# Optimization experiments

Measured on AMD Instinct MI355X. Metric: run time of the kernel, lower is better.

The kernel has to match this reference:

```python
import jax, jax.numpy as jnp
import numpy as np

B, S, D, H, DH = 2, 2048, 1024, 16, 64
LN_EPS = 1e-5

def _layernorm(x, g, b):
    mu = jnp.mean(x, axis=-1, keepdims=True)
    var = jnp.mean(jnp.square(x - mu), axis=-1, keepdims=True)
    return (x - mu) * jax.lax.rsqrt(var + LN_EPS) * g + b

def setup_inputs() -> dict:
    key = jax.random.key(0)
    ks = jax.random.split(key, 12)
    s = 0.02
    return {
        'x': jax.random.normal(ks[0], (B, S, D), jnp.float32),
        'attention_mask': jnp.zeros((B, S), jnp.bool_),
        'Wq': jax.random.normal(ks[1], (H, D, DH), jnp.float32) * s,
        'bq': jnp.zeros((H, DH), jnp.float32),
        'Wk': jax.random.normal(ks[2], (H, D, DH), jnp.float32) * s,
        'bk': jnp.zeros((H, DH), jnp.float32),
        'Wv': jax.random.normal(ks[3], (H, D, DH), jnp.float32) * s,
        'bv': jnp.zeros((H, DH), jnp.float32),
        'ln_g': jnp.ones((D,), jnp.float32),
        'ln_b': jnp.zeros((D,), jnp.float32),
        'W1': jax.random.normal(ks[4], (D, 4 * D), jnp.float32) * s,
        'b1': jnp.zeros((4 * D,), jnp.float32),
        'W2': jax.random.normal(ks[5], (4 * D, D), jnp.float32) * s,
        'b2': jnp.zeros((D,), jnp.float32),
    }

def reference(x, attention_mask, Wq, bq, Wk, bk, Wv, bv, ln_g, ln_b, W1, b1, W2, b2):
    # NOTE: source has a typo bug ('attentoin_score'), so the attention_mask is
    # computed-then-discarded; softmax is applied to the UNMASKED scaled scores.
    dh = Wq.shape[-1]
    q = jnp.einsum('bsd,hde->bhse', x, Wq) + bq[:, None, :]  # [B,H,S,dh]
    k = jnp.einsum('bsd,hde->bhse', x, Wk) + bk[:, None, :]
    v = jnp.einsum('bsd,hde->bhse', x, Wv) + bv[:, None, :]
    scores = jnp.einsum('bhse,bhte->bhst', q, k) / jnp.sqrt(jnp.float32(dh))
    attn = jax.nn.softmax(scores, axis=-1)
    o = jnp.einsum('bhst,bhte->bhse', attn, v)  # [B,H,S,dh]
    b_, h_, s_, e_ = o.shape
    # concat heads along last dim == transpose then reshape
    mha = jnp.transpose(o, (0, 2, 1, 3)).reshape(b_, s_, h_ * e_)
    h1 = _layernorm(x + mha, ln_g, ln_b)
    ffn = jax.nn.relu(h1 @ W1 + b1) @ W2 + b2
    return _layernorm(h1 + ffn, ln_g, ln_b)
```

## Files before the change

### kernel.cpp

```cpp
#include <hip/hip_runtime.h>

#define DEVI __device__ __forceinline__

typedef __attribute__((ext_vector_type(8))) __bf16 bf16x8;
typedef __attribute__((ext_vector_type(4))) float f32x4;
typedef __attribute__((ext_vector_type(4))) unsigned short u16x4;
typedef __attribute__((ext_vector_type(8))) unsigned short u16x8;

static DEVI unsigned short f2bf(float f) {
  unsigned int i = __float_as_uint(f);
  i += 0x7fffu + ((i >> 16) & 1u);
  return (unsigned short)(i >> 16);
}

static DEVI unsigned short f2bfh(float f) {
  union { __bf16 h; unsigned short u; } c;
  c.h = (__bf16)f;
  return c.u;
}

static DEVI f32x4 mfma16x16x32(bf16x8 a, bf16x8 b, f32x4 c) {
  return __builtin_amdgcn_mfma_f32_16x16x32_bf16(a, b, c, 0, 0, 0);
}

static DEVI void async_ld16(const void* g, void* lds) {
  __builtin_amdgcn_global_load_lds(
      (const __attribute__((address_space(1))) void*)g,
      (__attribute__((address_space(3))) void*)lds, 16, 0, 0);
}

template <int BN, int OUT_MODE, bool RELU>
static DEVI void gemm_bt_core(const unsigned short* __restrict__ A, int lda,
                              const unsigned short* __restrict__ Bt, int ldb,
                              int K, int m0, int n0,
                              const float* __restrict__ bias,
                              void* __restrict__ Cp, int ldc,
                              const float* __restrict__ bq,
                              const float* __restrict__ bk,
                              const float* __restrict__ bv,
                              unsigned short* __restrict__ qo,
                              unsigned short* __restrict__ ko,
                              unsigned short* __restrict__ vo) {
  constexpr int MT = (BN == 128) ? 4 : 2;
  constexpr int NT = 4;
  __shared__ __align__(16) unsigned short As[128 * 32];
  __shared__ __align__(16) unsigned short Bs[BN * 32];

  const int tid = threadIdx.x;
  const int w = tid >> 6, l = tid & 63;
  const int lr = l & 15, lq = l >> 4;
  const int wm0 = (BN == 128) ? ((w >> 1) * 64) : (w * 32);
  const int wn0 = (BN == 128) ? ((w & 1) * 64) : 0;
  const int lrow = l >> 2;
  const int lcol = (l & 3) * 8;

  f32x4 acc[MT][NT];
#pragma unroll
  for (int i = 0; i < MT; ++i)
#pragma unroll
    for (int j = 0; j < NT; ++j) acc[i][j] = (f32x4){0.f, 0.f, 0.f, 0.f};

  for (int kb = 0; kb < K; kb += 32) {
#pragma unroll
    for (int p = 0; p < 2; ++p) {
      const int r0 = p * 64 + w * 16;
      async_ld16(A + (size_t)(m0 + r0 + lrow) * lda + kb + lcol, As + r0 * 32);
    }
#pragma unroll
    for (int p = 0; p < BN / 64; ++p) {
      const int r0 = p * 64 + w * 16;
      async_ld16(Bt + (size_t)(n0 + r0 + lrow) * ldb + kb + lcol, Bs + r0 * 32);
    }
    __syncthreads();

    bf16x8 af[MT], bfr[NT];
#pragma unroll
    for (int mt = 0; mt < MT; ++mt)
      af[mt] = *(const bf16x8*)(As + (wm0 + mt * 16 + lr) * 32 + lq * 8);
#pragma unroll
    for (int nt = 0; nt < NT; ++nt)
      bfr[nt] = *(const bf16x8*)(Bs + (wn0 + nt * 16 + lr) * 32 + lq * 8);
#pragma unroll
    for (int mt = 0; mt < MT; ++mt)
#pragma unroll
      for (int nt = 0; nt < NT; ++nt)
        acc[mt][nt] = mfma16x16x32(af[mt], bfr[nt], acc[mt][nt]);
    __syncthreads();
  }

#pragma unroll
  for (int mt = 0; mt < MT; ++mt) {
    const int grow = m0 + wm0 + mt * 16 + lq * 4;
#pragma unroll
    for (int nt = 0; nt < NT; ++nt) {
      const int gcol = n0 + wn0 + nt * 16 + lr;
      if (OUT_MODE == 2) {
        const int which = gcol >> 10;
        const int h = (gcol >> 6) & 15;
        const int e = gcol & 63;
        const float* bp = (which == 0) ? bq : (which == 1) ? bk : bv;
        const float bvv = bp[gcol & 1023];
        unsigned short* op = (which == 0) ? qo : (which == 1) ? ko : vo;
#pragma unroll
        for (int r = 0; r < 4; ++r) {
          const int row = grow + r;
          const int b_ = row >> 11, s_ = row & 2047;
          const size_t base = (size_t)((b_ << 4) + h) * 131072 + (size_t)s_ * 64;
          if (which == 1) {
            const int o = e >> 3;
            const int pos = (((o ^ (s_ & 7)) << 3) | (e & 7));
            op[base + pos] = f2bf((acc[mt][nt][r] + bvv) * 0.18033688011112f);
          } else {
            op[base + e] = f2bf(acc[mt][nt][r] + bvv);
          }
        }
      } else if (OUT_MODE == 3) {
#pragma unroll
        for (int r = 0; r < 4; ++r)
          ((unsigned short*)Cp)[(size_t)(grow + r) * ldc + gcol] =
              f2bf(acc[mt][nt][r]);
      } else {
        const float bvv = bias[gcol];
#pragma unroll
        for (int r = 0; r < 4; ++r) {
          float val = acc[mt][nt][r] + bvv;
          if (RELU) val = fmaxf(val, 0.f);
          if (OUT_MODE == 1)
            ((unsigned short*)Cp)[(size_t)(grow + r) * ldc + gcol] = f2bf(val);
          else
            ((float*)Cp)[(size_t)(grow + r) * ldc + gcol] = val;
        }
      }
    }
  }
}

__global__ __launch_bounds__(256) void k_gemm_qkv(
    const unsigned short* __restrict__ xb, const unsigned short* __restrict__ Wt,
    const float* __restrict__ bq, const float* __restrict__ bk,
    const float* __restrict__ bv, unsigned short* __restrict__ qo,
    unsigned short* __restrict__ ko, unsigned short* __restrict__ vo) {
  gemm_bt_core<128, 2, false>(xb, 1024, Wt, 1024, 1024, blockIdx.x * 128,
                              blockIdx.y * 128, nullptr, nullptr, 0, bq, bk, bv,
                              qo, ko, vo);
}

__global__ __launch_bounds__(256) void k_ffn1(
    const unsigned short* __restrict__ h1b, const unsigned short* __restrict__ W1t,
    const float* __restrict__ b1, unsigned short* __restrict__ f1) {
  gemm_bt_core<128, 1, true>(h1b, 1024, W1t, 1024, 1024, blockIdx.x * 128,
                             blockIdx.y * 128, b1, f1, 4096, nullptr, nullptr,
                             nullptr, nullptr, nullptr, nullptr);
}

__global__ __launch_bounds__(256) void k_ffn2(
    const unsigned short* __restrict__ f1, const unsigned short* __restrict__ W2t,
    unsigned short* __restrict__ p0, unsigned short* __restrict__ p1) {
  const int z = blockIdx.z;
  unsigned short* p = z ? p1 : p0;
  gemm_bt_core<64, 3, false>(f1 + z * 2048, 4096, W2t + z * 2048, 4096, 2048,
                             blockIdx.x * 128, blockIdx.y * 64, nullptr, p, 1024,
                             nullptr, nullptr, nullptr, nullptr, nullptr,
                             nullptr);
}

__global__ __launch_bounds__(256) void k_cvt(const float* __restrict__ src,
                                             unsigned short* __restrict__ dst) {
  const size_t i = ((size_t)blockIdx.x * 256 + threadIdx.x) * 4;
  f32x4 v = *(const f32x4*)(src + i);
  u16x4 pk;
#pragma unroll
  for (int j = 0; j < 4; ++j) pk[j] = f2bf(v[j]);
  *(u16x4*)(dst + i) = pk;
}

static DEVI void tr64(const float* __restrict__ s, int sld,
                      unsigned short* __restrict__ d, int dld) {
  __shared__ float t[64][65];
  const int tr = threadIdx.x >> 4;
  const int tc4 = (threadIdx.x & 15) * 4;
#pragma unroll
  for (int i = 0; i < 4; ++i) {
    f32x4 v = *(const f32x4*)(s + (size_t)(i * 16 + tr) * sld + tc4);
#pragma unroll
    for (int j = 0; j < 4; ++j) t[i * 16 + tr][tc4 + j] = v[j];
  }
  __syncthreads();
#pragma unroll
  for (int i = 0; i < 4; ++i) {
    const int c = i * 16 + tr;
    u16x4 pk;
#pragma unroll
    for (int j = 0; j < 4; ++j) pk[j] = f2bf(t[tc4 + j][c]);
    *(u16x4*)(d + (size_t)c * dld + tc4) = pk;
  }
}

__global__ __launch_bounds__(256) void k_tw(const float* __restrict__ src,
                                            unsigned short* __restrict__ dst,
                                            int C) {
  const int R = (int)gridDim.x * 64;
  const int r0 = blockIdx.x * 64, c0 = blockIdx.y * 64;
  tr64(src + (size_t)r0 * C + c0, C, dst + (size_t)c0 * R + r0, R);
}

__global__ __launch_bounds__(256) void k_twqkv(const float* __restrict__ Wq,
                                               const float* __restrict__ Wk,
                                               const float* __restrict__ Wv,
                                               unsigned short* __restrict__ dst) {
  const int which = blockIdx.y >> 4, h = blockIdx.y & 15;
  const float* W = (which == 0) ? Wq : (which == 1) ? Wk : Wv;
  const float* s = W + (size_t)h * 65536;
  unsigned short* d = dst + (size_t)(which * 1024 + h * 64) * 1024;
  const int r0 = blockIdx.x * 64;
  tr64(s + (size_t)r0 * 64, 64, d + r0, 1024);
}

__global__ __launch_bounds__(256) void k_vprep(const unsigned short* __restrict__ vb,
                                               unsigned short* __restrict__ vp) {
  const int bh = blockIdx.y, t = blockIdx.x;
  __shared__ unsigned short tl[64][72];
  const int tid = threadIdx.x;
  const size_t base = (size_t)bh * 131072;
  const int kr = tid >> 3, oc = tid & 7;
#pragma unroll
  for (int p = 0; p < 2; ++p) {
    const int key = p * 32 + kr;
    *(u16x8*)&tl[key][oc * 8] =
        *(const u16x8*)(vb + base + (size_t)(t * 64 + key) * 64 + oc * 8);
  }
  __syncthreads();
#pragma unroll
  for (int p = 0; p < 2; ++p) {
    const int dh = p * 32 + kr;
    const int ok = oc ^ (dh & 7);
    u16x8 pk;
#pragma unroll
    for (int j = 0; j < 8; ++j) {
      const int kap = ok * 8 + j;
      const int key = (kap & 3) * 16 + (kap >> 2);
      pk[j] = tl[key][dh];
    }
    *(u16x8*)(vp + base + (size_t)dh * 2048 + t * 64 + oc * 8) = pk;
  }
}

__global__ __launch_bounds__(256) void k_attn(
    const unsigned short* __restrict__ q, const unsigned short* __restrict__ ks,
    const unsigned short* __restrict__ vp, float* __restrict__ mha) {
  const int bid = blockIdx.x;
  const int bh = (bid & 7) * 4 + ((bid >> 3) >> 4);
  const int qt = (bid >> 3) & 15;
  const int b = bh >> 4, h = bh & 15;
  const int tid = threadIdx.x;
  const int w = tid >> 6, l = tid & 63;
  const int lr = l & 15, lq = l >> 4, l7 = lr & 7;

  __shared__ __align__(16) unsigned short Ks[2][64 * 64];
  __shared__ __align__(16) unsigned short Vt[2][64 * 64];
  __shared__ __align__(16) unsigned short Ps[4][32][72];

  const size_t bho = (size_t)bh * 131072;
  const int q0 = qt * 128 + w * 32;

  bf16x8 qf[2][2];
#pragma unroll
  for (int mt = 0; mt < 2; ++mt) {
    const unsigned short* qp = q + bho + (size_t)(q0 + mt * 16 + lr) * 64 + lq * 8;
    qf[mt][0] = *(const bf16x8*)qp;
    qf[mt][1] = *(const bf16x8*)(qp + 32);
  }

  f32x4 l_acc[2][4];
  f32x4 o[2][4];
#pragma unroll
  for (int mt = 0; mt < 2; ++mt)
#pragma unroll
    for (int i = 0; i < 4; ++i) {
      l_acc[mt][i] = (f32x4){0.f, 0.f, 0.f, 0.f};
      o[mt][i] = (f32x4){0.f, 0.f, 0.f, 0.f};
    }

  const unsigned short* kg = ks + bho;
  const unsigned short* vg = vp + bho;
  const int srow = l >> 3, scol = (l & 7) * 8;

#pragma unroll
  for (int p = 0; p < 2; ++p) {
    const int r0 = w * 16 + p * 8;
    async_ld16(kg + (size_t)(r0 + srow) * 64 + scol, &Ks[0][r0 * 64]);
    async_ld16(vg + (size_t)(r0 + srow) * 2048 + scol, &Vt[0][r0 * 64]);
  }
  __syncthreads();

  for (int kt = 0; kt < 32; ++kt) {
    const int cur = kt & 1, nxt = cur ^ 1;
    if (kt + 1 < 32) {
      const int k1 = (kt + 1) * 64;
#pragma unroll
      for (int p = 0; p < 2; ++p) {
        const int r0 = w * 16 + p * 8;
        async_ld16(kg + (size_t)(k1 + r0 + srow) * 64 + scol, &Ks[nxt][r0 * 64]);
        async_ld16(vg + (size_t)(r0 + srow) * 2048 + k1 + scol, &Vt[nxt][r0 * 64]);
      }
    }

    bf16x8 kf[4][2];
#pragma unroll
    for (int ct = 0; ct < 4; ++ct)
#pragma unroll
      for (int hh = 0; hh < 2; ++hh)
        kf[ct][hh] = *(const bf16x8*)&Ks[cur][(ct * 16 + lr) * 64 +
                                             (((hh << 2) | lq) ^ l7) * 8];
    f32x4 s[2][4];
#pragma unroll
    for (int mt = 0; mt < 2; ++mt)
#pragma unroll
      for (int ct = 0; ct < 4; ++ct) {
        f32x4 t = {0.f, 0.f, 0.f, 0.f};
        t = mfma16x16x32(qf[mt][0], kf[ct][0], t);
        t = mfma16x16x32(qf[mt][1], kf[ct][1], t);
        s[mt][ct] = t;
      }

#pragma unroll
    for (int mt = 0; mt < 2; ++mt)
#pragma unroll
      for (int r = 0; r < 4; ++r) {
        f32x4 pe;
#pragma unroll
        for (int ct = 0; ct < 4; ++ct)
          pe[ct] = __builtin_amdgcn_exp2f(s[mt][ct][r]);
        l_acc[mt][r] += pe;
        u16x4 pk;
#pragma unroll
        for (int ct = 0; ct < 4; ++ct) pk[ct] = f2bfh(pe[ct]);
        *(u16x4*)&Ps[w][mt * 16 + lq * 4 + r][lr * 4] = pk;
      }
    __asm__ volatile("" ::: "memory");

    bf16x8 vf[4][2];
#pragma unroll
    for (int dt = 0; dt < 4; ++dt)
#pragma unroll
      for (int hh = 0; hh < 2; ++hh)
        vf[dt][hh] = *(const bf16x8*)&Vt[cur][(dt * 16 + lr) * 64 +
                                             (((hh << 2) | lq) ^ l7) * 8];
#pragma unroll
    for (int mt = 0; mt < 2; ++mt) {
      bf16x8 pf0 = *(const bf16x8*)&Ps[w][mt * 16 + lr][lq * 8];
      bf16x8 pf1 = *(const bf16x8*)&Ps[w][mt * 16 + lr][32 + lq * 8];
#pragma unroll
      for (int dt = 0; dt < 4; ++dt) {
        o[mt][dt] = mfma16x16x32(pf0, vf[dt][0], o[mt][dt]);
        o[mt][dt] = mfma16x16x32(pf1, vf[dt][1], o[mt][dt]);
      }
    }
    __syncthreads();
  }

#pragma unroll
  for (int mt = 0; mt < 2; ++mt)
#pragma unroll
    for (int r = 0; r < 4; ++r) {
      f32x4 la = l_acc[mt][r];
      float sd = la[0] + la[1] + la[2] + la[3];
      sd += __shfl_xor(sd, 1);
      sd += __shfl_xor(sd, 2);
      sd += __shfl_xor(sd, 4);
      sd += __shfl_xor(sd, 8);
      const float inv = 1.f / sd;
      float* op = mha + ((size_t)b * 2048 + q0 + mt * 16 + lq * 4 + r) * 1024 +
                  h * 64 + lr;
      op[0] = o[mt][0][r] * inv;
      op[16] = o[mt][1][r] * inv;
      op[32] = o[mt][2][r] * inv;
      op[48] = o[mt][3][r] * inv;
    }
}

__global__ __launch_bounds__(256) void k_add_ln(const float* __restrict__ a,
                                                const float* __restrict__ b,
                                                const float* __restrict__ g,
                                                const float* __restrict__ be,
                                                float* __restrict__ out,
                                                unsigned short* __restrict__ outb) {
  const int row = blockIdx.x;
  const int tid = threadIdx.x;
  const size_t base = (size_t)row * 1024 + tid * 4;
  f32x4 va = *(const f32x4*)(a + base);
  f32x4 vb = *(const f32x4*)(b + base);
  f32x4 xx;
  float s = 0.f, q = 0.f;
#pragma unroll
  for (int i = 0; i < 4; ++i) {
    xx[i] = va[i] + vb[i];
    s += xx[i];
    q += xx[i] * xx[i];
  }
#pragma unroll
  for (int off = 1; off < 64; off <<= 1) {
    s += __shfl_xor(s, off);
    q += __shfl_xor(q, off);
  }
  __shared__ float ss[4], qs[4];
  const int w = tid >> 6;
  if ((tid & 63) == 0) { ss[w] = s; qs[w] = q; }
  __syncthreads();
  s = ss[0] + ss[1] + ss[2] + ss[3];
  q = qs[0] + qs[1] + qs[2] + qs[3];
  const float mean = s * (1.f / 1024.f);
  const float var = q * (1.f / 1024.f) - mean * mean;
  const float rstd = rsqrtf(var + 1e-5f);
  f32x4 vg = *(const f32x4*)(g + tid * 4);
  f32x4 vbe = *(const f32x4*)(be + tid * 4);
  f32x4 ov;
#pragma unroll
  for (int i = 0; i < 4; ++i) ov[i] = (xx[i] - mean) * rstd * vg[i] + vbe[i];
  *(f32x4*)(out + base) = ov;
  if (outb) {
    u16x4 pk;
#pragma unroll
    for (int i = 0; i < 4; ++i) pk[i] = f2bf(ov[i]);
    *(u16x4*)(outb + base) = pk;
  }
}

__global__ __launch_bounds__(256) void k_add_ln3(
    const float* __restrict__ a, const unsigned short* __restrict__ p0,
    const unsigned short* __restrict__ p1, const float* __restrict__ cb,
    const float* __restrict__ g, const float* __restrict__ be,
    float* __restrict__ out) {
  const int row = blockIdx.x;
  const int tid = threadIdx.x;
  const size_t base = (size_t)row * 1024 + tid * 4;
  f32x4 va = *(const f32x4*)(a + base);
  u16x4 u0 = *(const u16x4*)(p0 + base);
  u16x4 u1 = *(const u16x4*)(p1 + base);
  f32x4 vcb = *(const f32x4*)(cb + tid * 4);
  f32x4 xx;
  float s = 0.f, q = 0.f;
#pragma unroll
  for (int i = 0; i < 4; ++i) {
    const float f0 = __uint_as_float((unsigned int)u0[i] << 16);
    const float f1 = __uint_as_float((unsigned int)u1[i] << 16);
    xx[i] = va[i] + f0 + f1 + vcb[i];
    s += xx[i];
    q += xx[i] * xx[i];
  }
#pragma unroll
  for (int off = 1; off < 64; off <<= 1) {
    s += __shfl_xor(s, off);
    q += __shfl_xor(q, off);
  }
  __shared__ float ss[4], qs[4];
  const int w = tid >> 6;
  if ((tid & 63) == 0) { ss[w] = s; qs[w] = q; }
  __syncthreads();
  s = ss[0] + ss[1] + ss[2] + ss[3];
  q = qs[0] + qs[1] + qs[2] + qs[3];
  const float mean = s * (1.f / 1024.f);
  const float var = q * (1.f / 1024.f) - mean * mean;
  const float rstd = rsqrtf(var + 1e-5f);
  f32x4 vg = *(const f32x4*)(g + tid * 4);
  f32x4 vbe = *(const f32x4*)(be + tid * 4);
  f32x4 ov;
#pragma unroll
  for (int i = 0; i < 4; ++i) ov[i] = (xx[i] - mean) * rstd * vg[i] + vbe[i];
  *(f32x4*)(out + base) = ov;
}

extern "C" void kernel_launch(void* const* d_in, const int* in_sizes, int n_in,
                              void* d_out, int out_size, void* d_ws,
                              size_t ws_size, hipStream_t stream) {
  const float* x = (const float*)d_in[0];
  const float* Wq = (const float*)d_in[2];
  const float* bq = (const float*)d_in[3];
  const float* Wk = (const float*)d_in[4];
  const float* bk = (const float*)d_in[5];
  const float* Wv = (const float*)d_in[6];
  const float* bv = (const float*)d_in[7];
  const float* lg = (const float*)d_in[8];
  const float* lb = (const float*)d_in[9];
  const float* W1 = (const float*)d_in[10];
  const float* b1 = (const float*)d_in[11];
  const float* W2 = (const float*)d_in[12];
  const float* b2 = (const float*)d_in[13];

  char* ws = (char*)d_ws;
  const size_t MB = 1024 * 1024;
  unsigned short* qb = (unsigned short*)(ws + 0);
  unsigned short* kb = (unsigned short*)(ws + 8 * MB);
  unsigned short* vb = (unsigned short*)(ws + 16 * MB);
  unsigned short* vp = (unsigned short*)(ws + 24 * MB);
  unsigned short* w2t = (unsigned short*)(ws + 0);
  unsigned short* f1 = (unsigned short*)(ws + 8 * MB);
  unsigned short* xb = (unsigned short*)(ws + 40 * MB);
  float* mha = (float*)(ws + 40 * MB);
  unsigned short* p1 = (unsigned short*)(ws + 40 * MB);
  float* h1 = (float*)(ws + 56 * MB);
  unsigned short* h1b = (unsigned short*)(ws + 72 * MB);
  unsigned short* p0 = (unsigned short*)(ws + 72 * MB);
  unsigned short* wqkvt = (unsigned short*)(ws + 80 * MB);
  unsigned short* w1t = (unsigned short*)(ws + 86 * MB);

  k_cvt<<<dim3(4096), 256, 0, stream>>>(x, xb);
  k_twqkv<<<dim3(16, 48), 256, 0, stream>>>(Wq, Wk, Wv, wqkvt);
  k_tw<<<dim3(16, 64), 256, 0, stream>>>(W1, w1t, 4096);

  k_gemm_qkv<<<dim3(32, 24), 256, 0, stream>>>(xb, wqkvt, bq, bk, bv, qb, kb, vb);
  k_vprep<<<dim3(32, 32), 256, 0, stream>>>(vb, vp);
  k_attn<<<dim3(512), 256, 0, stream>>>(qb, kb, vp, mha);

  k_tw<<<dim3(64, 16), 256, 0, stream>>>(W2, w2t, 1024);
  k_add_ln<<<dim3(4096), 256, 0, stream>>>(x, mha, lg, lb, h1, h1b);
  k_ffn1<<<dim3(32, 32), 256, 0, stream>>>(h1b, w1t, b1, f1);
  k_ffn2<<<dim3(32, 16, 2), 256, 0, stream>>>(f1, w2t, p0, p1);
  k_add_ln3<<<dim3(4096), 256, 0, stream>>>(h1, p0, p1, b2, lg, lb,
                                            (float*)d_out);
}
```

Baseline: 339.6 us.

## Split attention block into 8 waves each owning 16 query rows

The attention kernel now runs 512 threads (8 waves) per block instead of 256, and each wave handles one 16-row query tile instead of two. K/V tile loads are spread over 8 waves, so each thread issues one async load per tile instead of two. The aim is more waves for latency hiding and lower register pressure per wave. The cost is that each K/V fragment read from LDS now feeds half as many MFMAs, which raises LDS traffic per FLOP, and synchronisation is across more waves.

```diff
diff --git a/kernel.cpp b/kernel.cpp
--- a/kernel.cpp
+++ b/kernel.cpp
@@ -245,7 +245,7 @@
   }
 }
 
-__global__ __launch_bounds__(256) void k_attn(
+__global__ __launch_bounds__(512) void k_attn(
     const unsigned short* __restrict__ q, const unsigned short* __restrict__ ks,
     const unsigned short* __restrict__ vp, float* __restrict__ mha) {
   const int bid = blockIdx.x;
@@ -258,51 +258,41 @@
 
   __shared__ __align__(16) unsigned short Ks[2][64 * 64];
   __shared__ __align__(16) unsigned short Vt[2][64 * 64];
-  __shared__ __align__(16) unsigned short Ps[4][32][72];
+  __shared__ __align__(16) unsigned short Ps[8][16][72];
 
   const size_t bho = (size_t)bh * 131072;
-  const int q0 = qt * 128 + w * 32;
-
-  bf16x8 qf[2][2];
-#pragma unroll
-  for (int mt = 0; mt < 2; ++mt) {
-    const unsigned short* qp = q + bho + (size_t)(q0 + mt * 16 + lr) * 64 + lq * 8;
-    qf[mt][0] = *(const bf16x8*)qp;
-    qf[mt][1] = *(const bf16x8*)(qp + 32);
-  }
-
-  f32x4 l_acc[2][4];
-  f32x4 o[2][4];
-#pragma unroll
-  for (int mt = 0; mt < 2; ++mt)
-#pragma unroll
-    for (int i = 0; i < 4; ++i) {
-      l_acc[mt][i] = (f32x4){0.f, 0.f, 0.f, 0.f};
-      o[mt][i] = (f32x4){0.f, 0.f, 0.f, 0.f};
-    }
+  const int q0 = qt * 128 + w * 16;
+
+  bf16x8 qf0, qf1;
+  {
+    const unsigned short* qp = q + bho + (size_t)(q0 + lr) * 64 + lq * 8;
+    qf0 = *(const bf16x8*)qp;
+    qf1 = *(const bf16x8*)(qp + 32);
+  }
+
+  f32x4 l_acc[4];
+  f32x4 o[4];
+#pragma unroll
+  for (int i = 0; i < 4; ++i) {
+    l_acc[i] = (f32x4){0.f, 0.f, 0.f, 0.f};
+    o[i] = (f32x4){0.f, 0.f, 0.f, 0.f};
+  }
 
   const unsigned short* kg = ks + bho;
   const unsigned short* vg = vp + bho;
   const int srow = l >> 3, scol = (l & 7) * 8;
-
-#pragma unroll
-  for (int p = 0; p < 2; ++p) {
-    const int r0 = w * 16 + p * 8;
-    async_ld16(kg + (size_t)(r0 + srow) * 64 + scol, &Ks[0][r0 * 64]);
-    async_ld16(vg + (size_t)(r0 + srow) * 2048 + scol, &Vt[0][r0 * 64]);
-  }
+  const int r0 = w * 8;
+
+  async_ld16(kg + (size_t)(r0 + srow) * 64 + scol, &Ks[0][r0 * 64]);
+  async_ld16(vg + (size_t)(r0 + srow) * 2048 + scol, &Vt[0][r0 * 64]);
   __syncthreads();
 
   for (int kt = 0; kt < 32; ++kt) {
     const int cur = kt & 1, nxt = cur ^ 1;
     if (kt + 1 < 32) {
       const int k1 = (kt + 1) * 64;
-#pragma unroll
-      for (int p = 0; p < 2; ++p) {
-        const int r0 = w * 16 + p * 8;
-        async_ld16(kg + (size_t)(k1 + r0 + srow) * 64 + scol, &Ks[nxt][r0 * 64]);
-        async_ld16(vg + (size_t)(r0 + srow) * 2048 + k1 + scol, &Vt[nxt][r0 * 64]);
-      }
+      async_ld16(kg + (size_t)(k1 + r0 + srow) * 64 + scol, &Ks[nxt][r0 * 64]);
+      async_ld16(vg + (size_t)(r0 + srow) * 2048 + k1 + scol, &Vt[nxt][r0 * 64]);
     }
 
     bf16x8 kf[4][2];
@@ -312,31 +302,27 @@
       for (int hh = 0; hh < 2; ++hh)
         kf[ct][hh] = *(const bf16x8*)&Ks[cur][(ct * 16 + lr) * 64 +
                                              (((hh << 2) | lq) ^ l7) * 8];
-    f32x4 s[2][4];
-#pragma unroll
-    for (int mt = 0; mt < 2; ++mt)
-#pragma unroll
-      for (int ct = 0; ct < 4; ++ct) {
-        f32x4 t = {0.f, 0.f, 0.f, 0.f};
-        t = mfma16x16x32(qf[mt][0], kf[ct][0], t);
-        t = mfma16x16x32(qf[mt][1], kf[ct][1], t);
-        s[mt][ct] = t;
-      }
-
-#pragma unroll
-    for (int mt = 0; mt < 2; ++mt)
-#pragma unroll
-      for (int r = 0; r < 4; ++r) {
-        f32x4 pe;
-#pragma unroll
-        for (int ct = 0; ct < 4; ++ct)
-          pe[ct] = __builtin_amdgcn_exp2f(s[mt][ct][r]);
-        l_acc[mt][r] += pe;
-        u16x4 pk;
-#pragma unroll
-        for (int ct = 0; ct < 4; ++ct) pk[ct] = f2bfh(pe[ct]);
-        *(u16x4*)&Ps[w][mt * 16 + lq * 4 + r][lr * 4] = pk;
-      }
+    f32x4 s[4];
+#pragma unroll
+    for (int ct = 0; ct < 4; ++ct) {
+      f32x4 t = {0.f, 0.f, 0.f, 0.f};
+      t = mfma16x16x32(qf0, kf[ct][0], t);
+      t = mfma16x16x32(qf1, kf[ct][1], t);
+      s[ct] = t;
+    }
+
+#pragma unroll
+    for (int r = 0; r < 4; ++r) {
+      f32x4 pe;
+#pragma unroll
+      for (int ct = 0; ct < 4; ++ct)
+        pe[ct] = __builtin_amdgcn_exp2f(s[ct][r]);
+      l_acc[r] += pe;
+      u16x4 pk;
+#pragma unroll
+      for (int ct = 0; ct < 4; ++ct) pk[ct] = f2bfh(pe[ct]);
+      *(u16x4*)&Ps[w][lq * 4 + r][lr * 4] = pk;
+    }
     __asm__ volatile("" ::: "memory");
 
     bf16x8 vf[4][2];
@@ -346,37 +332,31 @@
       for (int hh = 0; hh < 2; ++hh)
         vf[dt][hh] = *(const bf16x8*)&Vt[cur][(dt * 16 + lr) * 64 +
                                              (((hh << 2) | lq) ^ l7) * 8];
-#pragma unroll
-    for (int mt = 0; mt < 2; ++mt) {
-      bf16x8 pf0 = *(const bf16x8*)&Ps[w][mt * 16 + lr][lq * 8];
-      bf16x8 pf1 = *(const bf16x8*)&Ps[w][mt * 16 + lr][32 + lq * 8];
-#pragma unroll
-      for (int dt = 0; dt < 4; ++dt) {
-        o[mt][dt] = mfma16x16x32(pf0, vf[dt][0], o[mt][dt]);
-        o[mt][dt] = mfma16x16x32(pf1, vf[dt][1], o[mt][dt]);
-      }
+    bf16x8 pf0 = *(const bf16x8*)&Ps[w][lr][lq * 8];
+    bf16x8 pf1 = *(const bf16x8*)&Ps[w][lr][32 + lq * 8];
+#pragma unroll
+    for (int dt = 0; dt < 4; ++dt) {
+      o[dt] = mfma16x16x32(pf0, vf[dt][0], o[dt]);
+      o[dt] = mfma16x16x32(pf1, vf[dt][1], o[dt]);
     }
     __syncthreads();
   }
 
 #pragma unroll
-  for (int mt = 0; mt < 2; ++mt)
-#pragma unroll
-    for (int r = 0; r < 4; ++r) {
-      f32x4 la = l_acc[mt][r];
-      float sd = la[0] + la[1] + la[2] + la[3];
-      sd += __shfl_xor(sd, 1);
-      sd += __shfl_xor(sd, 2);
-      sd += __shfl_xor(sd, 4);
-      sd += __shfl_xor(sd, 8);
-      const float inv = 1.f / sd;
-      float* op = mha + ((size_t)b * 2048 + q0 + mt * 16 + lq * 4 + r) * 1024 +
-                  h * 64 + lr;
-      op[0] = o[mt][0][r] * inv;
-      op[16] = o[mt][1][r] * inv;
-      op[32] = o[mt][2][r] * inv;
-      op[48] = o[mt][3][r] * inv;
-    }
+  for (int r = 0; r < 4; ++r) {
+    f32x4 la = l_acc[r];
+    float sd = la[0] + la[1] + la[2] + la[3];
+    sd += __shfl_xor(sd, 1);
+    sd += __shfl_xor(sd, 2);
+    sd += __shfl_xor(sd, 4);
+    sd += __shfl_xor(sd, 8);
+    const float inv = 1.f / sd;
+    float* op = mha + ((size_t)b * 2048 + q0 + lq * 4 + r) * 1024 + h * 64 + lr;
+    op[0] = o[0][r] * inv;
+    op[16] = o[1][r] * inv;
+    op[32] = o[2][r] * inv;
+    op[48] = o[3][r] * inv;
+  }
 }
 
 __global__ __launch_bounds__(256) void k_add_ln(const float* __restrict__ a,
@@ -510,7 +490,7 @@
 
   k_gemm_qkv<<<dim3(32, 24), 256, 0, stream>>>(xb, wqkvt, bq, bk, bv, qb, kb, vb);
   k_vprep<<<dim3(32, 32), 256, 0, stream>>>(vb, vp);
-  k_attn<<<dim3(512), 256, 0, stream>>>(qb, kb, vp, mha);
+  k_attn<<<dim3(512), 512, 0, stream>>>(qb, kb, vp, mha);
 
   k_tw<<<dim3(64, 16), 256, 0, stream>>>(W2, w2t, 1024);
   k_add_ln<<<dim3(4096), 256, 0, stream>>>(x, mha, lg, lb, h1, h1b);
```

Result: faster. 329.1 us (-3.1%).
